# Performance work log

Hardware: AMD Instinct MI355X
Metric: run time of the kernel (lower is better)

Reference implementation:

```python
import jax, jax.numpy as jnp
import numpy as np

N_NODES = 100000
N_FEAT = 512
HIDDEN = 16
OUT = 2
N_EDGES = 3200000


def gcn_conv(x, edge_index, W, b, n_nodes):
    """PyG-style GCNConv: h = D^-1/2 (A+I) D^-1/2 (x W) + b."""
    h = x @ W  # project first (PyG order) -> [N, out]
    src, dst = edge_index[0], edge_index[1]
    # add self loops
    loop = jnp.arange(n_nodes, dtype=src.dtype)
    src = jnp.concatenate([src, loop])
    dst = jnp.concatenate([dst, loop])
    # symmetric normalization: deg = in-degree (scatter ones to dst)
    deg = jax.ops.segment_sum(jnp.ones_like(dst, dtype=h.dtype), dst, num_segments=n_nodes)
    dinv = jax.lax.rsqrt(deg)  # deg >= 1 due to self loops
    norm = dinv[src] * dinv[dst]  # [E+N]
    msg = h[src] * norm[:, None]  # gather + scale
    out = jax.ops.segment_sum(msg, dst, num_segments=n_nodes)  # scatter-add
    return out + b


def setup_inputs() -> dict:
    key = jax.random.key(0)
    k1, k2, k3, k4, k5 = jax.random.split(key, 5)
    x = jax.random.normal(k1, (N_NODES, N_FEAT), dtype=jnp.float32)
    edge_index = jax.random.randint(k2, (2, N_EDGES), 0, N_NODES, dtype=jnp.int64)
    # Glorot-style params for the two GCNConv layers
    W1 = jax.random.normal(k3, (N_FEAT, HIDDEN), dtype=jnp.float32) / np.sqrt(N_FEAT)
    b1 = jnp.zeros((HIDDEN,), dtype=jnp.float32)
    W2 = jax.random.normal(k4, (HIDDEN, OUT), dtype=jnp.float32) / np.sqrt(HIDDEN)
    b2 = jnp.zeros((OUT,), dtype=jnp.float32)
    return {"x": x, "edge_index": edge_index, "W1": W1, "b1": b1, "W2": W2, "b2": b2}


def reference(x, edge_index, W1, b1, W2, b2):
    n = x.shape[0]
    h = gcn_conv(x, edge_index, W1, b1, n)
    h = jax.nn.relu(h)
    out = gcn_conv(h, edge_index, W2, b2, n)
    return out
```

## Files before the change

### kernel.cpp

```cpp
#include <hip/hip_runtime.h>
#include <hip/hip_fp16.h>

#define NFEAT 512
#define HID 16
#define MAXNB 512
#define NBLK 512
#define PACK_SHIFT 17
#define PACK_MASK ((1 << PACK_SHIFT) - 1)

typedef _Float16 f16x8 __attribute__((ext_vector_type(8)));
typedef float f32x4 __attribute__((ext_vector_type(4)));

__device__ __forceinline__ void gemm_tile(const float* __restrict__ x,
                                          const float* __restrict__ W,
                                          __half* __restrict__ h1u,
                                          int tile, int N, int lane) {
  const int n = lane & 15;
  const int g = lane >> 4;

  f16x8 bf[16];
#pragma unroll
  for (int f = 0; f < 16; ++f) {
    const float* wp = W + (size_t)(f * 32 + g * 8) * HID + n;
#pragma unroll
    for (int j = 0; j < 8; ++j) bf[f][j] = (_Float16)wp[j * HID];
  }

  int rowbase = tile * 16;
  if (rowbase + 16 > N) rowbase = N - 16;
  const float* xr = x + (size_t)(rowbase + n) * NFEAT + g * 8;

  f32x4 acc = {0.f, 0.f, 0.f, 0.f};
#pragma unroll
  for (int f = 0; f < 16; ++f) {
    float4 p0 = *(const float4*)(xr + f * 32);
    float4 p1 = *(const float4*)(xr + f * 32 + 4);
    f16x8 af;
    af[0] = (_Float16)p0.x; af[1] = (_Float16)p0.y;
    af[2] = (_Float16)p0.z; af[3] = (_Float16)p0.w;
    af[4] = (_Float16)p1.x; af[5] = (_Float16)p1.y;
    af[6] = (_Float16)p1.z; af[7] = (_Float16)p1.w;
    acc = __builtin_amdgcn_mfma_f32_16x16x32_f16(af, bf[f], acc, 0, 0, 0);
  }

#pragma unroll
  for (int r = 0; r < 4; ++r) {
    int row = rowbase + g * 4 + r;
    h1u[(size_t)row * HID + n] = __float2half(acc[r]);
  }
}

__global__ __launch_bounds__(512) void k_hist_gemm(const int* __restrict__ ei,
                                                   int* __restrict__ cnt_t,
                                                   int E, int nb,
                                                   const float* __restrict__ x,
                                                   const float* __restrict__ W,
                                                   __half* __restrict__ h1u,
                                                   int N, int tsplit) {
  __shared__ int l[MAXNB];
  if (blockIdx.x < NBLK) {
    for (int i = threadIdx.x; i < nb; i += 512) l[i] = 0;
    __syncthreads();
    int chunk = (E + NBLK - 1) / NBLK;
    int beg = blockIdx.x * chunk;
    int end = beg + chunk; if (end > E) end = E;
    for (int e = beg + threadIdx.x; e < end; e += 512)
      atomicAdd(&l[ei[(size_t)E + e] >> 8], 1);
    __syncthreads();
    for (int b = threadIdx.x; b < nb; b += 512)
      cnt_t[(size_t)b * NBLK + blockIdx.x] = l[b];
  } else {
    int tile = (blockIdx.x - NBLK) * 8 + (threadIdx.x >> 6);
    if (tile < tsplit) gemm_tile(x, W, h1u, tile, N, threadIdx.x & 63);
  }
}

__global__ __launch_bounds__(512) void k_scan(const int* __restrict__ cnt_t,
                                              int* __restrict__ off_t,
                                              int* __restrict__ gcnt, int nb) {
  int b = blockIdx.x * 8 + (threadIdx.x >> 6);
  if (b >= nb) return;
  int lane = threadIdx.x & 63;
  int4 v0 = *(const int4*)&cnt_t[(size_t)b * NBLK + lane * 8];
  int4 v1 = *(const int4*)&cnt_t[(size_t)b * NBLK + lane * 8 + 4];
  int tot = (v0.x + v0.y + v0.z + v0.w) + (v1.x + v1.y + v1.z + v1.w);
  int s = tot;
  for (int d = 1; d < 64; d <<= 1) {
    int o = __shfl_up(s, d);
    if (lane >= d) s += o;
  }
  int excl = s - tot;
  int4 w0, w1;
  w0.x = excl;
  w0.y = w0.x + v0.x;
  w0.z = w0.y + v0.y;
  w0.w = w0.z + v0.z;
  w1.x = w0.w + v0.w;
  w1.y = w1.x + v1.x;
  w1.z = w1.y + v1.y;
  w1.w = w1.z + v1.z;
  *(int4*)&off_t[(size_t)b * NBLK + lane * 8] = w0;
  *(int4*)&off_t[(size_t)b * NBLK + lane * 8 + 4] = w1;
  if (lane == 63) gcnt[b] = s;
}

__device__ __forceinline__ void bscan_lds(const int* __restrict__ gcnt, int nb,
                                          int* sm , int& my_pc) {
  int t = threadIdx.x;
  int c = (t < nb) ? gcnt[t] : 0;
  my_pc = (c + 15) & ~15;
  sm[t] = my_pc;
  __syncthreads();
  for (int off = 1; off < 512; off <<= 1) {
    int x = (t >= off) ? sm[t - off] : 0;
    __syncthreads();
    sm[t] += x;
    __syncthreads();
  }
}

__global__ __launch_bounds__(512) void k_scatter_gemm(const int* __restrict__ ei,
                                                      const int* __restrict__ gcnt,
                                                      const int* __restrict__ off_t,
                                                      int* __restrict__ binned,
                                                      int E, int nb,
                                                      const float* __restrict__ x,
                                                      const float* __restrict__ W,
                                                      __half* __restrict__ h1u,
                                                      int N, int tsplit, int ntiles) {
  __shared__ int cur[MAXNB];
  __shared__ int sm[512];
  if (blockIdx.x < NBLK) {
    int my_pc;
    bscan_lds(gcnt, nb, sm, my_pc);
    int t = threadIdx.x;
    if (t < nb) cur[t] = (sm[t] - my_pc) + off_t[(size_t)t * NBLK + blockIdx.x];
    __syncthreads();
    int chunk = (E + NBLK - 1) / NBLK;
    int beg = blockIdx.x * chunk;
    int end = beg + chunk; if (end > E) end = E;
    for (int e = beg + threadIdx.x; e < end; e += 512) {
      int s = ei[e];
      int d = ei[(size_t)E + e];
      int b = d >> 8;
      int pos = atomicAdd(&cur[b], 1);
      binned[pos] = s | ((d & 255) << PACK_SHIFT);
    }
  } else {
    int tile = tsplit + (blockIdx.x - NBLK) * 8 + (threadIdx.x >> 6);
    if (tile < ntiles) gemm_tile(x, W, h1u, tile, N, threadIdx.x & 63);
  }
}

__global__ __launch_bounds__(512) void k_sortbucket(const int* __restrict__ gcnt,
                                                    const int* __restrict__ binned,
                                                    int* __restrict__ csr,
                                                    int* __restrict__ rowbeg,
                                                    int* __restrict__ rowend,
                                                    float* __restrict__ dinv,
                                                    __half* __restrict__ h1h,
                                                    int nb, int N) {
  __shared__ int smg[512];
  __shared__ int hist[256];
  __shared__ int sm[256];
  __shared__ int cur[256];
  __shared__ float sdinv[256];
  __shared__ int sbase;
  const int t = threadIdx.x;
  const int b = blockIdx.x;
  {
    int my_pc;
    bscan_lds(gcnt, nb, smg, my_pc);
    if (t == b) sbase = smg[t] - my_pc;
    __syncthreads();
  }
  const int base = sbase;
  const int cnt = gcnt[b];
  if (t < 256) hist[t] = 0;
  __syncthreads();
  for (int j = base + t; j < base + cnt; j += 512)
    atomicAdd(&hist[binned[j] >> PACK_SHIFT], 1);
  __syncthreads();
  int h = 0;
  if (t < 256) {
    h = hist[t];
    sm[t] = h;
  }
  __syncthreads();
  for (int off = 1; off < 256; off <<= 1) {
    int x = 0;
    if (t < 256 && t >= off) x = sm[t - off];
    __syncthreads();
    if (t < 256) sm[t] += x;
    __syncthreads();
  }
  if (t < 256) {
    int incl = sm[t];
    int excl = incl - h;
    cur[t] = excl;
    float dv = rsqrtf((float)h + 1.0f);
    sdinv[t] = dv;
    int node = b * 256 + t;
    if (node < N) {
      rowbeg[node] = base + excl;
      rowend[node] = base + incl;
      dinv[node] = dv;
    }
  }
  __syncthreads();
  for (int j = base + t; j < base + cnt; j += 512) {
    int val = binned[j];
    int pos = atomicAdd(&cur[val >> PACK_SHIFT], 1);
    csr[base + pos] = val & PACK_MASK;
  }
  {
    int node = b * 256 + (t >> 1);
    if (node < N) {
      float dv = sdinv[t >> 1];
      __half* hp = h1h + (size_t)node * HID + (t & 1) * 8;
      f16x8 v = *(const f16x8*)hp;
#pragma unroll
      for (int j = 0; j < 8; ++j) v[j] = (_Float16)((float)v[j] * dv);
      *(f16x8*)hp = v;
    }
  }
}

__global__ __launch_bounds__(256) void k_agg1f(const int* __restrict__ rowbeg,
                                               const int* __restrict__ rowend,
                                               const int* __restrict__ csr,
                                               const __half* __restrict__ h1h,
                                               const float* __restrict__ dinv,
                                               const float* __restrict__ b1,
                                               const float* __restrict__ W2,
                                               float* __restrict__ h2s, int N) {
  const int f = threadIdx.x & 15;
  const int node = blockIdx.x * 16 + (threadIdx.x >> 4);
  if (node >= N) return;
  int j = rowbeg[node];
  const int end = rowend[node];
  float acc = __half2float(h1h[(size_t)node * HID + f]);
  for (; j < end && (j & 3); ++j) acc += __half2float(h1h[(size_t)csr[j] * HID + f]);
  for (; j + 8 <= end; j += 8) {
    int4 s0 = *(const int4*)&csr[j];
    int4 s1 = *(const int4*)&csr[j + 4];
    float a0 = __half2float(h1h[(size_t)s0.x * HID + f]);
    float a1 = __half2float(h1h[(size_t)s0.y * HID + f]);
    float a2 = __half2float(h1h[(size_t)s0.z * HID + f]);
    float a3 = __half2float(h1h[(size_t)s0.w * HID + f]);
    float a4 = __half2float(h1h[(size_t)s1.x * HID + f]);
    float a5 = __half2float(h1h[(size_t)s1.y * HID + f]);
    float a6 = __half2float(h1h[(size_t)s1.z * HID + f]);
    float a7 = __half2float(h1h[(size_t)s1.w * HID + f]);
    acc += ((a0 + a1) + (a2 + a3)) + ((a4 + a5) + (a6 + a7));
  }
  for (; j + 4 <= end; j += 4) {
    int4 ss = *(const int4*)&csr[j];
    float a0 = __half2float(h1h[(size_t)ss.x * HID + f]);
    float a1 = __half2float(h1h[(size_t)ss.y * HID + f]);
    float a2 = __half2float(h1h[(size_t)ss.z * HID + f]);
    float a3 = __half2float(h1h[(size_t)ss.w * HID + f]);
    acc += (a0 + a1) + (a2 + a3);
  }
  for (; j < end; ++j) acc += __half2float(h1h[(size_t)csr[j] * HID + f]);

  float di = dinv[node];
  float v = fmaxf(acc * di + b1[f], 0.f);
  float o0 = v * W2[f * 2 + 0];
  float o1 = v * W2[f * 2 + 1];
#pragma unroll
  for (int d = 1; d < 16; d <<= 1) {
    o0 += __shfl_xor(o0, d);
    o1 += __shfl_xor(o1, d);
  }
  if (f == 0) *(float2*)&h2s[(size_t)node * 2] = make_float2(o0 * di, o1 * di);
}

__global__ __launch_bounds__(256) void k_agg2f(const int* __restrict__ rowbeg,
                                               const int* __restrict__ rowend,
                                               const int* __restrict__ csr,
                                               const float* __restrict__ h2s,
                                               const float* __restrict__ dinv,
                                               const float* __restrict__ b2,
                                               float* __restrict__ out, int N) {
  const int l = threadIdx.x & 3;
  const int node = blockIdx.x * 64 + (threadIdx.x >> 2);
  if (node >= N) return;
  const int beg = rowbeg[node];
  const int end = rowend[node];
  float ox = 0.f, oy = 0.f;
  for (int j = beg + l; j < end; j += 4) {
    int s = csr[j];
    float2 v = *(const float2*)&h2s[(size_t)s * 2];
    ox += v.x;
    oy += v.y;
  }
  ox += __shfl_xor(ox, 1); oy += __shfl_xor(oy, 1);
  ox += __shfl_xor(ox, 2); oy += __shfl_xor(oy, 2);
  if (l == 0) {
    float2 self = *(const float2*)&h2s[(size_t)node * 2];
    float di = dinv[node];
    float2 o;
    o.x = (ox + self.x) * di + b2[0];
    o.y = (oy + self.y) * di + b2[1];
    *(float2*)&out[(size_t)node * 2] = o;
  }
}

extern "C" void kernel_launch(void* const* d_in, const int* in_sizes, int n_in,
                              void* d_out, int out_size, void* d_ws, size_t ws_size,
                              hipStream_t stream) {
  const float* x = (const float*)d_in[0];
  const int* ei = (const int*)d_in[1];
  const float* W1 = (const float*)d_in[2];
  const float* b1 = (const float*)d_in[3];
  const float* W2 = (const float*)d_in[4];
  const float* b2 = (const float*)d_in[5];
  float* out = (float*)d_out;
  const int N = in_sizes[0] / NFEAT;
  const int E = in_sizes[1] / 2;
  const int nb = (N + 255) / 256;

  char* p = (char*)d_ws;
  int* cnt_t = (int*)p;    p += (size_t)MAXNB * NBLK * 4;
  int* off_t = (int*)p;    p += (size_t)MAXNB * NBLK * 4;
  int* gcnt = (int*)p;     p += (size_t)MAXNB * 4;
  int* binned = (int*)p;   p += ((size_t)E + MAXNB * 16) * 4;
  int* csr = (int*)p;      p += ((size_t)E + MAXNB * 16) * 4;
  int* rowbeg = (int*)p;   p += (size_t)N * 4;
  int* rowend = (int*)p;   p += (size_t)N * 4;
  float* dinv = (float*)p; p += (size_t)N * 4;
  __half* h1h = (__half*)p; p += (size_t)N * HID * 2;
  float* h2s = (float*)p;  p += (size_t)N * 2 * 4;

  const int ntiles = (N + 15) / 16;
  const int tsplit = ((ntiles / 2) + 7) & ~7;
  const int gA = (tsplit + 7) / 8;
  const int gB = (ntiles - tsplit + 7) / 8;

  k_hist_gemm<<<NBLK + gA, 512, 0, stream>>>(ei, cnt_t, E, nb, x, W1, h1h, N, tsplit);
  k_scan<<<(nb + 7) / 8, 512, 0, stream>>>(cnt_t, off_t, gcnt, nb);
  k_scatter_gemm<<<NBLK + gB, 512, 0, stream>>>(ei, gcnt, off_t, binned, E, nb,
                                                x, W1, h1h, N, tsplit, ntiles);
  k_sortbucket<<<nb, 512, 0, stream>>>(gcnt, binned, csr, rowbeg, rowend,
                                       dinv, h1h, nb, N);
  k_agg1f<<<(N + 15) / 16, 256, 0, stream>>>(rowbeg, rowend, csr, h1h, dinv, b1, W2, h2s, N);
  k_agg2f<<<(N + 63) / 64, 256, 0, stream>>>(rowbeg, rowend, csr, h2s, dinv, b2, out, N);
}
```

Baseline: 170.3 us.

## Split GEMM across three graph-build kernels and apply source dinv during aggregation

```diff
diff --git a/kernel.cpp b/kernel.cpp
--- a/kernel.cpp
+++ b/kernel.cpp
@@ -56,7 +56,7 @@
                                                    const float* __restrict__ x,
                                                    const float* __restrict__ W,
                                                    __half* __restrict__ h1u,
-                                                   int N, int tsplit) {
+                                                   int N, int t1) {
   __shared__ int l[MAXNB];
   if (blockIdx.x < NBLK) {
     for (int i = threadIdx.x; i < nb; i += 512) l[i] = 0;
@@ -71,7 +71,7 @@
       cnt_t[(size_t)b * NBLK + blockIdx.x] = l[b];
   } else {
     int tile = (blockIdx.x - NBLK) * 8 + (threadIdx.x >> 6);
-    if (tile < tsplit) gemm_tile(x, W, h1u, tile, N, threadIdx.x & 63);
+    if (tile < t1) gemm_tile(x, W, h1u, tile, N, threadIdx.x & 63);
   }
 }
 
@@ -127,7 +127,7 @@
                                                       const float* __restrict__ x,
                                                       const float* __restrict__ W,
                                                       __half* __restrict__ h1u,
-                                                      int N, int tsplit, int ntiles) {
+                                                      int N, int t1, int t2) {
   __shared__ int cur[MAXNB];
   __shared__ int sm[512];
   if (blockIdx.x < NBLK) {
@@ -147,27 +147,34 @@
       binned[pos] = s | ((d & 255) << PACK_SHIFT);
     }
   } else {
-    int tile = tsplit + (blockIdx.x - NBLK) * 8 + (threadIdx.x >> 6);
-    if (tile < ntiles) gemm_tile(x, W, h1u, tile, N, threadIdx.x & 63);
-  }
-}
-
-__global__ __launch_bounds__(512) void k_sortbucket(const int* __restrict__ gcnt,
-                                                    const int* __restrict__ binned,
-                                                    int* __restrict__ csr,
-                                                    int* __restrict__ rowbeg,
-                                                    int* __restrict__ rowend,
-                                                    float* __restrict__ dinv,
-                                                    __half* __restrict__ h1h,
-                                                    int nb, int N) {
+    int tile = t1 + (blockIdx.x - NBLK) * 8 + (threadIdx.x >> 6);
+    if (tile < t2) gemm_tile(x, W, h1u, tile, N, threadIdx.x & 63);
+  }
+}
+
+__global__ __launch_bounds__(512) void k_sort_gemm(const int* __restrict__ gcnt,
+                                                   const int* __restrict__ binned,
+                                                   int* __restrict__ csr,
+                                                   int* __restrict__ rowbeg,
+                                                   int* __restrict__ rowend,
+                                                   float* __restrict__ dinv,
+                                                   int nb, int N,
+                                                   const float* __restrict__ x,
+                                                   const float* __restrict__ W,
+                                                   __half* __restrict__ h1u,
+                                                   int t2, int ntiles) {
   __shared__ int smg[512];
   __shared__ int hist[256];
   __shared__ int sm[256];
   __shared__ int cur[256];
-  __shared__ float sdinv[256];
   __shared__ int sbase;
   const int t = threadIdx.x;
   const int b = blockIdx.x;
+  if (b >= nb) {
+    int tile = t2 + (b - nb) * 8 + (t >> 6);
+    if (tile < ntiles) gemm_tile(x, W, h1u, tile, N, t & 63);
+    return;
+  }
   {
     int my_pc;
     bscan_lds(gcnt, nb, smg, my_pc);
@@ -188,23 +195,21 @@
   }
   __syncthreads();
   for (int off = 1; off < 256; off <<= 1) {
-    int x = 0;
-    if (t < 256 && t >= off) x = sm[t - off];
-    __syncthreads();
-    if (t < 256) sm[t] += x;
+    int x2 = 0;
+    if (t < 256 && t >= off) x2 = sm[t - off];
+    __syncthreads();
+    if (t < 256) sm[t] += x2;
     __syncthreads();
   }
   if (t < 256) {
     int incl = sm[t];
     int excl = incl - h;
     cur[t] = excl;
-    float dv = rsqrtf((float)h + 1.0f);
-    sdinv[t] = dv;
     int node = b * 256 + t;
     if (node < N) {
       rowbeg[node] = base + excl;
       rowend[node] = base + incl;
-      dinv[node] = dv;
+      dinv[node] = rsqrtf((float)h + 1.0f);
     }
   }
   __syncthreads();
@@ -213,23 +218,12 @@
     int pos = atomicAdd(&cur[val >> PACK_SHIFT], 1);
     csr[base + pos] = val & PACK_MASK;
   }
-  {
-    int node = b * 256 + (t >> 1);
-    if (node < N) {
-      float dv = sdinv[t >> 1];
-      __half* hp = h1h + (size_t)node * HID + (t & 1) * 8;
-      f16x8 v = *(const f16x8*)hp;
-#pragma unroll
-      for (int j = 0; j < 8; ++j) v[j] = (_Float16)((float)v[j] * dv);
-      *(f16x8*)hp = v;
-    }
-  }
 }
 
 __global__ __launch_bounds__(256) void k_agg1f(const int* __restrict__ rowbeg,
                                                const int* __restrict__ rowend,
                                                const int* __restrict__ csr,
-                                               const __half* __restrict__ h1h,
+                                               const __half* __restrict__ h1u,
                                                const float* __restrict__ dinv,
                                                const float* __restrict__ b1,
                                                const float* __restrict__ W2,
@@ -239,32 +233,40 @@
   if (node >= N) return;
   int j = rowbeg[node];
   const int end = rowend[node];
-  float acc = __half2float(h1h[(size_t)node * HID + f]);
-  for (; j < end && (j & 3); ++j) acc += __half2float(h1h[(size_t)csr[j] * HID + f]);
+  const float di = dinv[node];
+  float acc = __half2float(h1u[(size_t)node * HID + f]) * di;
+  for (; j < end && (j & 3); ++j) {
+    int s = csr[j];
+    acc += __half2float(h1u[(size_t)s * HID + f]) * dinv[s];
+  }
   for (; j + 8 <= end; j += 8) {
     int4 s0 = *(const int4*)&csr[j];
     int4 s1 = *(const int4*)&csr[j + 4];
-    float a0 = __half2float(h1h[(size_t)s0.x * HID + f]);
-    float a1 = __half2float(h1h[(size_t)s0.y * HID + f]);
-    float a2 = __half2float(h1h[(size_t)s0.z * HID + f]);
-    float a3 = __half2float(h1h[(size_t)s0.w * HID + f]);
-    float a4 = __half2float(h1h[(size_t)s1.x * HID + f]);
-    float a5 = __half2float(h1h[(size_t)s1.y * HID + f]);
-    float a6 = __half2float(h1h[(size_t)s1.z * HID + f]);
-    float a7 = __half2float(h1h[(size_t)s1.w * HID + f]);
+    float d0 = dinv[s0.x], d1 = dinv[s0.y], d2 = dinv[s0.z], d3 = dinv[s0.w];
+    float d4 = dinv[s1.x], d5 = dinv[s1.y], d6 = dinv[s1.z], d7 = dinv[s1.w];
+    float a0 = __half2float(h1u[(size_t)s0.x * HID + f]) * d0;
+    float a1 = __half2float(h1u[(size_t)s0.y * HID + f]) * d1;
+    float a2 = __half2float(h1u[(size_t)s0.z * HID + f]) * d2;
+    float a3 = __half2float(h1u[(size_t)s0.w * HID + f]) * d3;
+    float a4 = __half2float(h1u[(size_t)s1.x * HID + f]) * d4;
+    float a5 = __half2float(h1u[(size_t)s1.y * HID + f]) * d5;
+    float a6 = __half2float(h1u[(size_t)s1.z * HID + f]) * d6;
+    float a7 = __half2float(h1u[(size_t)s1.w * HID + f]) * d7;
     acc += ((a0 + a1) + (a2 + a3)) + ((a4 + a5) + (a6 + a7));
   }
   for (; j + 4 <= end; j += 4) {
     int4 ss = *(const int4*)&csr[j];
-    float a0 = __half2float(h1h[(size_t)ss.x * HID + f]);
-    float a1 = __half2float(h1h[(size_t)ss.y * HID + f]);
-    float a2 = __half2float(h1h[(size_t)ss.z * HID + f]);
-    float a3 = __half2float(h1h[(size_t)ss.w * HID + f]);
+    float a0 = __half2float(h1u[(size_t)ss.x * HID + f]) * dinv[ss.x];
+    float a1 = __half2float(h1u[(size_t)ss.y * HID + f]) * dinv[ss.y];
+    float a2 = __half2float(h1u[(size_t)ss.z * HID + f]) * dinv[ss.z];
+    float a3 = __half2float(h1u[(size_t)ss.w * HID + f]) * dinv[ss.w];
     acc += (a0 + a1) + (a2 + a3);
   }
-  for (; j < end; ++j) acc += __half2float(h1h[(size_t)csr[j] * HID + f]);
-
-  float di = dinv[node];
+  for (; j < end; ++j) {
+    int s = csr[j];
+    acc += __half2float(h1u[(size_t)s * HID + f]) * dinv[s];
+  }
+
   float v = fmaxf(acc * di + b1[f], 0.f);
   float o0 = v * W2[f * 2 + 0];
   float o1 = v * W2[f * 2 + 1];
@@ -330,20 +332,22 @@
   int* rowbeg = (int*)p;   p += (size_t)N * 4;
   int* rowend = (int*)p;   p += (size_t)N * 4;
   float* dinv = (float*)p; p += (size_t)N * 4;
-  __half* h1h = (__half*)p; p += (size_t)N * HID * 2;
+  __half* h1u = (__half*)p; p += (size_t)N * HID * 2;
   float* h2s = (float*)p;  p += (size_t)N * 2 * 4;
 
   const int ntiles = (N + 15) / 16;
-  const int tsplit = ((ntiles / 2) + 7) & ~7;
-  const int gA = (tsplit + 7) / 8;
-  const int gB = (ntiles - tsplit + 7) / 8;
-
-  k_hist_gemm<<<NBLK + gA, 512, 0, stream>>>(ei, cnt_t, E, nb, x, W1, h1h, N, tsplit);
+  const int t1 = ((ntiles / 3) + 7) & ~7;
+  const int t2 = ((2 * ntiles / 3) + 7) & ~7;
+  const int gA = (t1 + 7) / 8;
+  const int gB = (t2 - t1 + 7) / 8;
+  const int gC = (ntiles - t2 + 7) / 8;
+
+  k_hist_gemm<<<NBLK + gA, 512, 0, stream>>>(ei, cnt_t, E, nb, x, W1, h1u, N, t1);
   k_scan<<<(nb + 7) / 8, 512, 0, stream>>>(cnt_t, off_t, gcnt, nb);
   k_scatter_gemm<<<NBLK + gB, 512, 0, stream>>>(ei, gcnt, off_t, binned, E, nb,
-                                                x, W1, h1h, N, tsplit, ntiles);
-  k_sortbucket<<<nb, 512, 0, stream>>>(gcnt, binned, csr, rowbeg, rowend,
-                                       dinv, h1h, nb, N);
-  k_agg1f<<<(N + 15) / 16, 256, 0, stream>>>(rowbeg, rowend, csr, h1h, dinv, b1, W2, h2s, N);
+                                                x, W1, h1u, N, t1, t2);
+  k_sort_gemm<<<nb + gC, 512, 0, stream>>>(gcnt, binned, csr, rowbeg, rowend,
+                                           dinv, nb, N, x, W1, h1u, t2, ntiles);
+  k_agg1f<<<(N + 15) / 16, 256, 0, stream>>>(rowbeg, rowend, csr, h1u, dinv, b1, W2, h2s, N);
   k_agg2f<<<(N + 63) / 64, 256, 0, stream>>>(rowbeg, rowend, csr, h2s, dinv, b2, out, N);
 }
```

New measurement: 182.7 us. 1.07x slower.
